# Kernel tuning notes

Hardware: AMD Instinct MI355X
Metric: run time of the kernel (lower is better)

## Reference

```python
import jax, jax.numpy as jnp
import numpy as np

D_MODEL = 64
N_HEAD = 4
HEAD_DIM = D_MODEL // N_HEAD  # 16


def setup_inputs() -> dict:
    key = jax.random.key(0)
    ks = jax.random.split(key, 8)
    B, T_dec, T_enc = 16, 1024, 1024
    s = 1.0 / np.sqrt(D_MODEL)
    return {
        "x": jax.random.normal(ks[0], (B, T_dec, D_MODEL), dtype=jnp.float32),
        "encoder_outputs": jax.random.normal(ks[1], (B, T_enc, D_MODEL), dtype=jnp.float32),
        "encoder_outputs_mask": jnp.ones((B, T_enc), dtype=jnp.int32),
        "Wkv": jax.random.normal(ks[2], (D_MODEL, 2 * D_MODEL), dtype=jnp.float32) * s,
        "bkv": jnp.zeros((2 * D_MODEL,), dtype=jnp.float32),
        "Wq": jax.random.normal(ks[3], (D_MODEL, D_MODEL), dtype=jnp.float32) * s,
        "bq": jnp.zeros((D_MODEL,), dtype=jnp.float32),
        "Wproj": jax.random.normal(ks[4], (D_MODEL, D_MODEL), dtype=jnp.float32) * s,
        "bproj": jnp.zeros((D_MODEL,), dtype=jnp.float32),
    }


def reference(x, encoder_outputs, encoder_outputs_mask, Wkv, bkv, Wq, bq, Wproj, bproj):
    B, T_dec, C = x.shape
    T_enc = encoder_outputs.shape[1]
    kv = encoder_outputs @ Wkv + bkv                      # [B, T_enc, 2C]
    k, v = kv[..., :D_MODEL], kv[..., D_MODEL:]          # [B, T_enc, C]
    q = x @ Wq + bq                                      # [B, T_dec, C]
    q = q.reshape(B, T_dec, N_HEAD, HEAD_DIM)
    k = k.reshape(B, T_enc, N_HEAD, HEAD_DIM)
    v = v.reshape(B, T_enc, N_HEAD, HEAD_DIM)
    scale = 1.0 / jnp.sqrt(jnp.asarray(HEAD_DIM, dtype=q.dtype))
    att = jnp.einsum("bqhd,bkhd->bhqk", q, k) * scale    # [B, H, T_dec, T_enc]
    mask = (encoder_outputs_mask == 0)[:, None, None, :]  # [B, 1, 1, T_enc]
    att = jnp.where(mask, jnp.asarray(-jnp.inf, dtype=att.dtype), att)
    att = jax.nn.softmax(att, axis=-1)
    ctx = jnp.einsum("bhqk,bkhd->bqhd", att, v).reshape(B, T_dec, C)
    # dropout is identity at eval time
    return ctx @ Wproj + bproj
```

## Files before the change

kernel.cpp:

```cpp
#include <hip/hip_runtime.h>
#include <hip/hip_bf16.h>
#include <math.h>

#define DM 64
#define NH 4
#define HD 16
#define BATCH 16
#define TSEQ 1024

typedef short bf16x8 __attribute__((ext_vector_type(8)));
typedef float f32x16 __attribute__((ext_vector_type(16)));

static __device__ inline short f2bf(float x) {
    __hip_bfloat16 h = __float2bfloat16(x);
    return __builtin_bit_cast(short, h);
}
static __device__ inline float bf2f(short s) {
    __hip_bfloat16 h = __builtin_bit_cast(__hip_bfloat16, s);
    return __bfloat162float(h);
}
static __device__ inline unsigned pack2bf(float a, float b) {
    const unsigned lo = (unsigned short)f2bf(a);
    const unsigned hi = (unsigned short)f2bf(b);
    return lo | (hi << 16);
}

__global__ __launch_bounds__(256) void proj_kernel(
    const float* __restrict__ x, const float* __restrict__ enc,
    const float* __restrict__ Wkv, const float* __restrict__ bkv,
    const float* __restrict__ Wq,  const float* __restrict__ bq,
    const int* __restrict__ mask,
    short* __restrict__ qhi, short* __restrict__ qlo,
    short* __restrict__ khi, short* __restrict__ klo,
    short* __restrict__ vtt)
{
    const int t = threadIdx.x;
    const int part = blockIdx.y;
    const int r0 = blockIdx.x * 512 + t;

    const float* in; const float* W; const float* bias; int cb, ldw;
    if (part < 4)      { in = x;   W = Wq;  ldw = 64;  cb = part*16;          bias = bq;  }
    else if (part < 8) { in = enc; W = Wkv; ldw = 128; cb = (part-4)*16;      bias = bkv; }
    else               { in = enc; W = Wkv; ldw = 128; cb = 64 + (part-8)*16; bias = bkv; }

    const float4* row0 = (const float4*)(in + (size_t)r0 * 64);
    const float4* row1 = (const float4*)(in + (size_t)(r0 + 256) * 64);

    float4 xc[2][4];
    #pragma unroll
    for (int v4 = 0; v4 < 4; ++v4) { xc[0][v4] = row0[v4]; xc[1][v4] = row1[v4]; }

    __shared__ float wsl[64][16];
    #pragma unroll
    for (int idx = t; idx < 1024; idx += 256)
        wsl[idx >> 4][idx & 15] = W[(idx >> 4)*ldw + cb + (idx & 15)];
    __syncthreads();

    float acc[2][16];
    #pragma unroll
    for (int j = 0; j < 16; ++j) { float bj = bias[cb + j]; acc[0][j] = bj; acc[1][j] = bj; }

    for (int kc = 0; kc < 4; ++kc) {
        float4 xn[2][4];
        if (kc < 3) {
            #pragma unroll
            for (int v4 = 0; v4 < 4; ++v4) {
                xn[0][v4] = row0[(kc+1)*4 + v4];
                xn[1][v4] = row1[(kc+1)*4 + v4];
            }
        }
        #pragma unroll
        for (int i = 0; i < 16; ++i) {
            const int k = kc*16 + i;
            const float4 w0 = ((const float4*)&wsl[k][0])[0];
            const float4 w1 = ((const float4*)&wsl[k][0])[1];
            const float4 w2 = ((const float4*)&wsl[k][0])[2];
            const float4 w3 = ((const float4*)&wsl[k][0])[3];
            #pragma unroll
            for (int rr = 0; rr < 2; ++rr) {
                const float xv = ((const float*)&xc[rr][i >> 2])[i & 3];
                acc[rr][0]  += xv*w0.x; acc[rr][1]  += xv*w0.y; acc[rr][2]  += xv*w0.z; acc[rr][3]  += xv*w0.w;
                acc[rr][4]  += xv*w1.x; acc[rr][5]  += xv*w1.y; acc[rr][6]  += xv*w1.z; acc[rr][7]  += xv*w1.w;
                acc[rr][8]  += xv*w2.x; acc[rr][9]  += xv*w2.y; acc[rr][10] += xv*w2.z; acc[rr][11] += xv*w2.w;
                acc[rr][12] += xv*w3.x; acc[rr][13] += xv*w3.y; acc[rr][14] += xv*w3.z; acc[rr][15] += xv*w3.w;
            }
        }
        if (kc < 3) {
            #pragma unroll
            for (int v4 = 0; v4 < 4; ++v4) { xc[0][v4] = xn[0][v4]; xc[1][v4] = xn[1][v4]; }
        }
    }

    #pragma unroll
    for (int rr = 0; rr < 2; ++rr) {
        const int r = r0 + rr*256;
        const int b = r >> 10, trow = r & 1023;
        if (part < 8) {
            const float scale = (part < 4) ? 0.36067376022224085f : 1.0f;
            short* dh = (part < 4) ? qhi : khi;
            short* dl = (part < 4) ? qlo : klo;
            const int h = (part < 4) ? part : (part - 4);
            bf16x8 h0, h1, l0, l1;
            #pragma unroll
            for (int j = 0; j < 16; ++j) {
                float vf = acc[rr][j] * scale;
                short hb = f2bf(vf);
                short lb = f2bf(vf - bf2f(hb));
                if (j < 8) { h0[j] = hb; l0[j] = lb; }
                else       { h1[j-8] = hb; l1[j-8] = lb; }
            }
            size_t off = (((size_t)(b*NH + h))*TSEQ + trow)*HD;
            *(bf16x8*)(dh + off)     = h0;
            *(bf16x8*)(dh + off + 8) = h1;
            *(bf16x8*)(dl + off)     = l0;
            *(bf16x8*)(dl + off + 8) = l1;
        } else {
            const int h = part - 8;
            const float mb = (mask[b*TSEQ + trow] != 0) ? 1.0f : 0.0f;
            short* tile = vtt + ((size_t)(b*NH + h))*32768 + (size_t)(trow >> 5)*1024;
            const int kw = trow & 31;
            #pragma unroll
            for (int j = 0; j < 16; ++j)
                tile[j*32 + kw] = f2bf(acc[rr][j] * mb);
            tile[16*32 + kw] = (mb != 0.0f) ? (short)0x3F80 : (short)0;
        }
    }
}

__global__ __launch_bounds__(512) void attn_kernel(
    const short* __restrict__ qhi, const short* __restrict__ qlo,
    const short* __restrict__ khi, const short* __restrict__ klo,
    const short* __restrict__ vtt,
    const float* __restrict__ Wproj, const float* __restrict__ bproj,
    float* __restrict__ out)
{
    const int tid  = threadIdx.x;
    const int lane = tid & 63;
    const int wid  = __builtin_amdgcn_readfirstlane(tid >> 6);
    const int h  = wid & 3;
    const int ks = wid >> 2;
    const int qbase = blockIdx.x * 32;
    const int b  = blockIdx.y;
    const int l31 = lane & 31;
    const bool hf = (lane >> 5) != 0;

    __shared__ float Cbuf[2][32][67];
    __shared__ float Lbuf[2][NH][32];

    const size_t qoff = (((size_t)(b*NH + h))*TSEQ + qbase + l31)*HD + (hf ? 8 : 0);
    const bf16x8 qBh = *(const bf16x8*)(qhi + qoff);
    const bf16x8 qBl = *(const bf16x8*)(qlo + qoff);

    const short* khb = khi + (((size_t)(b*NH + h))*TSEQ + ks*512)*HD;
    const short* klb = klo + (((size_t)(b*NH + h))*TSEQ + ks*512)*HD;
    const short* vtb = vtt + ((size_t)(b*NH + h))*32768 + (size_t)ks*16384;

    f32x16 Cacc;
    #pragma unroll
    for (int i = 0; i < 16; ++i) Cacc[i] = 0.f;

    for (int step = 0; step < 16; ++step) {
        const int ko = step * 32;
        const bf16x8 kAh = *(const bf16x8*)(khb + (size_t)(ko + l31)*HD + (hf ? 8 : 0));
        const bf16x8 kAl = *(const bf16x8*)(klb + (size_t)(ko + l31)*HD + (hf ? 8 : 0));
        const short* tile = vtb + (size_t)step * 1024;
        const bf16x8 vA0 = *(const bf16x8*)(tile + l31*32 + (hf ? 8 : 0));
        const bf16x8 vA1 = *(const bf16x8*)(tile + l31*32 + 16 + (hf ? 8 : 0));

        f32x16 S;
        #pragma unroll
        for (int i = 0; i < 16; ++i) S[i] = 0.f;
        S = __builtin_amdgcn_mfma_f32_32x32x16_bf16(kAh, qBh, S, 0, 0, 0);
        S = __builtin_amdgcn_mfma_f32_32x32x16_bf16(kAh, qBl, S, 0, 0, 0);
        S = __builtin_amdgcn_mfma_f32_32x32x16_bf16(kAl, qBh, S, 0, 0, 0);

        float p[16];
        #pragma unroll
        for (int i = 0; i < 16; ++i) p[i] = __builtin_amdgcn_exp2f(S[i]);

        unsigned pk[8];
        #pragma unroll
        for (int i = 0; i < 8; ++i) pk[i] = pack2bf(p[2*i], p[2*i+1]);

        const unsigned sA = hf ? pk[0] : pk[2];
        const unsigned sB = hf ? pk[1] : pk[3];
        const unsigned sC = hf ? pk[4] : pk[6];
        const unsigned sD = hf ? pk[5] : pk[7];
        const unsigned rA = (unsigned)__shfl_xor((int)sA, 32);
        const unsigned rB = (unsigned)__shfl_xor((int)sB, 32);
        const unsigned rC = (unsigned)__shfl_xor((int)sC, 32);
        const unsigned rD = (unsigned)__shfl_xor((int)sD, 32);

        int4 b1, b2;
        b1.x = hf ? (int)rA    : (int)pk[0];
        b1.y = hf ? (int)rB    : (int)pk[1];
        b1.z = hf ? (int)pk[2] : (int)rA;
        b1.w = hf ? (int)pk[3] : (int)rB;
        b2.x = hf ? (int)rC    : (int)pk[4];
        b2.y = hf ? (int)rD    : (int)pk[5];
        b2.z = hf ? (int)pk[6] : (int)rC;
        b2.w = hf ? (int)pk[7] : (int)rD;
        const bf16x8 pB0 = __builtin_bit_cast(bf16x8, b1);
        const bf16x8 pB1 = __builtin_bit_cast(bf16x8, b2);

        Cacc = __builtin_amdgcn_mfma_f32_32x32x16_bf16(vA0, pB0, Cacc, 0, 0, 0);
        Cacc = __builtin_amdgcn_mfma_f32_32x32x16_bf16(vA1, pB1, Cacc, 0, 0, 0);
    }

    #pragma unroll
    for (int r = 0; r < 8; ++r) {
        const int d = (r & 3) + 8*(r >> 2) + (hf ? 4 : 0);
        Cbuf[ks][l31][h*HD + d] = Cacc[r];
    }
    if (!hf) Lbuf[ks][h][l31] = Cacc[8];
    __syncthreads();

    const int q   = tid >> 4;
    const int cbo = (tid & 15) * 4;
    float linv[NH];
    #pragma unroll
    for (int hh = 0; hh < NH; ++hh)
        linv[hh] = 1.0f / (Lbuf[0][hh][q] + Lbuf[1][hh][q]);

    float o0 = bproj[cbo], o1 = bproj[cbo+1], o2 = bproj[cbo+2], o3 = bproj[cbo+3];
    #pragma unroll
    for (int i = 0; i < 64; ++i) {
        const float cv = (Cbuf[0][q][i] + Cbuf[1][q][i]) * linv[i >> 4];
        const float4 wr = *(const float4*)(Wproj + i*DM + cbo);
        o0 += cv*wr.x; o1 += cv*wr.y; o2 += cv*wr.z; o3 += cv*wr.w;
    }
    float4 st; st.x = o0; st.y = o1; st.z = o2; st.w = o3;
    *(float4*)(out + ((size_t)b*TSEQ + qbase + q)*DM + cbo) = st;
}

extern "C" void kernel_launch(void* const* d_in, const int* in_sizes, int n_in,
                              void* d_out, int out_size, void* d_ws, size_t ws_size,
                              hipStream_t stream) {
    const float* x     = (const float*)d_in[0];
    const float* enc   = (const float*)d_in[1];
    const int*   mask  = (const int*)  d_in[2];
    const float* Wkv   = (const float*)d_in[3];
    const float* bkv   = (const float*)d_in[4];
    const float* Wq    = (const float*)d_in[5];
    const float* bq    = (const float*)d_in[6];
    const float* Wproj = (const float*)d_in[7];
    const float* bproj = (const float*)d_in[8];
    float* out = (float*)d_out;

    const size_t SZ = (size_t)BATCH*NH*TSEQ*HD;
    short* qhi = (short*)d_ws;
    short* qlo = qhi + SZ;
    short* khi = qlo + SZ;
    short* klo = khi + SZ;
    short* vtt = klo + SZ;

    proj_kernel<<<dim3(32, 12), dim3(256), 0, stream>>>(
        x, enc, Wkv, bkv, Wq, bq, mask, qhi, qlo, khi, klo, vtt);
    attn_kernel<<<dim3(32, 16), dim3(512), 0, stream>>>(
        qhi, qlo, khi, klo, vtt, Wproj, bproj, out);
}
```

Measured before the change: 114.3 us.

## Drop Q low-part MFMA, prefetch K/V tiles, remap blocks to XCDs, inline bf16 rounding

Q is now stored only as a single bf16 value, so the score computation uses two MFMAs per step instead of three. The K and V fragments for the next step are loaded one iteration ahead, so their global latency overlaps with the current MFMA and exp work. The grid becomes 1D with a block-to-(batch, query) mapping that keeps each batch on a single XCD for L2 reuse. The bf16 conversions are replaced by hand-written round-to-nearest-even bit operations. Dropping the Q low part lowers score precision, and the prefetch adds register pressure.

```diff
diff --git a/kernel.cpp b/kernel.cpp
--- a/kernel.cpp
+++ b/kernel.cpp
@@ -11,18 +11,19 @@
 typedef short bf16x8 __attribute__((ext_vector_type(8)));
 typedef float f32x16 __attribute__((ext_vector_type(16)));
 
+static __device__ inline unsigned bfround(float x) {
+    unsigned u = __builtin_bit_cast(unsigned, x);
+    return u + 0x7fffu + ((u >> 16) & 1u);
+}
 static __device__ inline short f2bf(float x) {
-    __hip_bfloat16 h = __float2bfloat16(x);
-    return __builtin_bit_cast(short, h);
+    return (short)(bfround(x) >> 16);
 }
 static __device__ inline float bf2f(short s) {
-    __hip_bfloat16 h = __builtin_bit_cast(__hip_bfloat16, s);
-    return __bfloat162float(h);
+    unsigned u = ((unsigned)(unsigned short)s) << 16;
+    return __builtin_bit_cast(float, u);
 }
 static __device__ inline unsigned pack2bf(float a, float b) {
-    const unsigned lo = (unsigned short)f2bf(a);
-    const unsigned hi = (unsigned short)f2bf(b);
-    return lo | (hi << 16);
+    return (bfround(a) >> 16) | (bfround(b) & 0xffff0000u);
 }
 
 __global__ __launch_bounds__(256) void proj_kernel(
@@ -30,7 +31,7 @@
     const float* __restrict__ Wkv, const float* __restrict__ bkv,
     const float* __restrict__ Wq,  const float* __restrict__ bq,
     const int* __restrict__ mask,
-    short* __restrict__ qhi, short* __restrict__ qlo,
+    short* __restrict__ qws,
     short* __restrict__ khi, short* __restrict__ klo,
     short* __restrict__ vtt)
 {
@@ -95,25 +96,34 @@
     for (int rr = 0; rr < 2; ++rr) {
         const int r = r0 + rr*256;
         const int b = r >> 10, trow = r & 1023;
-        if (part < 8) {
-            const float scale = (part < 4) ? 0.36067376022224085f : 1.0f;
-            short* dh = (part < 4) ? qhi : khi;
-            short* dl = (part < 4) ? qlo : klo;
-            const int h = (part < 4) ? part : (part - 4);
+        if (part < 4) {
+            const float scale = 0.36067376022224085f;
+            const int h = part;
+            bf16x8 h0, h1;
+            #pragma unroll
+            for (int j = 0; j < 16; ++j) {
+                short hb = f2bf(acc[rr][j] * scale);
+                if (j < 8) h0[j] = hb; else h1[j-8] = hb;
+            }
+            size_t off = (((size_t)(b*NH + h))*TSEQ + trow)*HD;
+            *(bf16x8*)(qws + off)     = h0;
+            *(bf16x8*)(qws + off + 8) = h1;
+        } else if (part < 8) {
+            const int h = part - 4;
             bf16x8 h0, h1, l0, l1;
             #pragma unroll
             for (int j = 0; j < 16; ++j) {
-                float vf = acc[rr][j] * scale;
+                float vf = acc[rr][j];
                 short hb = f2bf(vf);
                 short lb = f2bf(vf - bf2f(hb));
                 if (j < 8) { h0[j] = hb; l0[j] = lb; }
                 else       { h1[j-8] = hb; l1[j-8] = lb; }
             }
             size_t off = (((size_t)(b*NH + h))*TSEQ + trow)*HD;
-            *(bf16x8*)(dh + off)     = h0;
-            *(bf16x8*)(dh + off + 8) = h1;
-            *(bf16x8*)(dl + off)     = l0;
-            *(bf16x8*)(dl + off + 8) = l1;
+            *(bf16x8*)(khi + off)     = h0;
+            *(bf16x8*)(khi + off + 8) = h1;
+            *(bf16x8*)(klo + off)     = l0;
+            *(bf16x8*)(klo + off + 8) = l1;
         } else {
             const int h = part - 8;
             const float mb = (mask[b*TSEQ + trow] != 0) ? 1.0f : 0.0f;
@@ -128,7 +138,7 @@
 }
 
 __global__ __launch_bounds__(512) void attn_kernel(
-    const short* __restrict__ qhi, const short* __restrict__ qlo,
+    const short* __restrict__ qws,
     const short* __restrict__ khi, const short* __restrict__ klo,
     const short* __restrict__ vtt,
     const float* __restrict__ Wproj, const float* __restrict__ bproj,
@@ -139,8 +149,11 @@
     const int wid  = __builtin_amdgcn_readfirstlane(tid >> 6);
     const int h  = wid & 3;
     const int ks = wid >> 2;
-    const int qbase = blockIdx.x * 32;
-    const int b  = blockIdx.y;
+    const int bid  = blockIdx.x;
+    const int xcd  = bid & 7;
+    const int slot = bid >> 3;
+    const int b    = (slot & 1) * 8 + xcd;
+    const int qbase = (slot >> 1) * 32;
     const int l31 = lane & 31;
     const bool hf = (lane >> 5) != 0;
 
@@ -148,8 +161,7 @@
     __shared__ float Lbuf[2][NH][32];
 
     const size_t qoff = (((size_t)(b*NH + h))*TSEQ + qbase + l31)*HD + (hf ? 8 : 0);
-    const bf16x8 qBh = *(const bf16x8*)(qhi + qoff);
-    const bf16x8 qBl = *(const bf16x8*)(qlo + qoff);
+    const bf16x8 qB = *(const bf16x8*)(qws + qoff);
 
     const short* khb = khi + (((size_t)(b*NH + h))*TSEQ + ks*512)*HD;
     const short* klb = klo + (((size_t)(b*NH + h))*TSEQ + ks*512)*HD;
@@ -159,20 +171,24 @@
     #pragma unroll
     for (int i = 0; i < 16; ++i) Cacc[i] = 0.f;
 
+    bf16x8 kAh = *(const bf16x8*)(khb + (size_t)l31*HD + (hf ? 8 : 0));
+    bf16x8 kAl = *(const bf16x8*)(klb + (size_t)l31*HD + (hf ? 8 : 0));
+    bf16x8 vA0 = *(const bf16x8*)(vtb + l31*32 + (hf ? 8 : 0));
+    bf16x8 vA1 = *(const bf16x8*)(vtb + l31*32 + 16 + (hf ? 8 : 0));
+
     for (int step = 0; step < 16; ++step) {
-        const int ko = step * 32;
-        const bf16x8 kAh = *(const bf16x8*)(khb + (size_t)(ko + l31)*HD + (hf ? 8 : 0));
-        const bf16x8 kAl = *(const bf16x8*)(klb + (size_t)(ko + l31)*HD + (hf ? 8 : 0));
-        const short* tile = vtb + (size_t)step * 1024;
-        const bf16x8 vA0 = *(const bf16x8*)(tile + l31*32 + (hf ? 8 : 0));
-        const bf16x8 vA1 = *(const bf16x8*)(tile + l31*32 + 16 + (hf ? 8 : 0));
+        const int nko = ((step < 15) ? step + 1 : 15) * 32;
+        const short* ntile = vtb + (size_t)(nko >> 5) * 1024;
+        const bf16x8 nkAh = *(const bf16x8*)(khb + (size_t)(nko + l31)*HD + (hf ? 8 : 0));
+        const bf16x8 nkAl = *(const bf16x8*)(klb + (size_t)(nko + l31)*HD + (hf ? 8 : 0));
+        const bf16x8 nvA0 = *(const bf16x8*)(ntile + l31*32 + (hf ? 8 : 0));
+        const bf16x8 nvA1 = *(const bf16x8*)(ntile + l31*32 + 16 + (hf ? 8 : 0));
 
         f32x16 S;
         #pragma unroll
         for (int i = 0; i < 16; ++i) S[i] = 0.f;
-        S = __builtin_amdgcn_mfma_f32_32x32x16_bf16(kAh, qBh, S, 0, 0, 0);
-        S = __builtin_amdgcn_mfma_f32_32x32x16_bf16(kAh, qBl, S, 0, 0, 0);
-        S = __builtin_amdgcn_mfma_f32_32x32x16_bf16(kAl, qBh, S, 0, 0, 0);
+        S = __builtin_amdgcn_mfma_f32_32x32x16_bf16(kAh, qB, S, 0, 0, 0);
+        S = __builtin_amdgcn_mfma_f32_32x32x16_bf16(kAl, qB, S, 0, 0, 0);
 
         float p[16];
         #pragma unroll
@@ -205,6 +221,8 @@
 
         Cacc = __builtin_amdgcn_mfma_f32_32x32x16_bf16(vA0, pB0, Cacc, 0, 0, 0);
         Cacc = __builtin_amdgcn_mfma_f32_32x32x16_bf16(vA1, pB1, Cacc, 0, 0, 0);
+
+        kAh = nkAh; kAl = nkAl; vA0 = nvA0; vA1 = nvA1;
     }
 
     #pragma unroll
@@ -248,14 +266,13 @@
     float* out = (float*)d_out;
 
     const size_t SZ = (size_t)BATCH*NH*TSEQ*HD;
-    short* qhi = (short*)d_ws;
-    short* qlo = qhi + SZ;
-    short* khi = qlo + SZ;
+    short* qws = (short*)d_ws;
+    short* khi = qws + SZ;
     short* klo = khi + SZ;
     short* vtt = klo + SZ;
 
     proj_kernel<<<dim3(32, 12), dim3(256), 0, stream>>>(
-        x, enc, Wkv, bkv, Wq, bq, mask, qhi, qlo, khi, klo, vtt);
-    attn_kernel<<<dim3(32, 16), dim3(512), 0, stream>>>(
-        qhi, qlo, khi, klo, vtt, Wproj, bproj, out);
-}
+        x, enc, Wkv, bkv, Wq, bq, mask, qws, khi, klo, vtt);
+    attn_kernel<<<dim3(512), dim3(512), 0, stream>>>(
+        qws, khi, klo, vtt, Wproj, bproj, out);
+}
```

New measurement: 113.9 us. Within noise of the previous version (-0.3%).
